# Kernel optimization log

Hardware: AMD Instinct MI355X
Metric: run time of the kernel (lower is better)

## Reference

```python
import jax, jax.numpy as jnp
import numpy as np

jax.config.update("jax_enable_x64", True)

STRIDE = 1
PADDING = 1


def _im2col(x, k, s):
    # x: (n, c, H, W) already padded. Returns (n, c*k*k, oh*ow) with
    # channel-major, then (kh, kw) ordering -- matching torch unfold/img2col.
    n, c, H, W = x.shape
    oh = (H - k) // s + 1
    ow = (W - k) // s + 1
    # k*k = 9 slices: small fixed loop over kernel offsets, fully vectorized
    # over batch/channel/spatial dims.
    patches = jnp.stack(
        [x[:, :, i:i + s * (oh - 1) + 1:s, j:j + s * (ow - 1) + 1:s]
         for i in range(k) for j in range(k)],
        axis=2,
    )  # (n, c, k*k, oh, ow)
    return patches.reshape(n, c * k * k, oh * ow)


def setup_inputs() -> dict:
    key = jax.random.key(0)
    k1, k2, k3 = jax.random.split(key, 3)
    x = jax.random.randint(k1, (32, 64, 56, 56), 0, 65536, dtype=jnp.int64)
    weight = jax.random.randint(k2, (64, 64, 3, 3), 0, 65536, dtype=jnp.int64)
    bias = jax.random.randint(k3, (64,), 0, 65536, dtype=jnp.int64)
    return {"x": x, "weight": weight, "bias": bias}


def reference(x, weight, bias):
    kN, kC, k, _ = weight.shape
    n, c, H, W = x.shape
    oh = (H - k + 2 * PADDING) // STRIDE + 1
    ow = (W - k + 2 * PADDING) // STRIDE + 1
    # pad spatial dims with zeros (ring zero)
    xp = jnp.pad(x, ((0, 0), (0, 0), (PADDING, PADDING), (PADDING, PADDING)))
    cols = _im2col(xp, k, STRIDE)              # (n, c*k*k, L)
    cols_t = cols.transpose(0, 2, 1)           # (n, L, c*k*k)
    w2 = weight.reshape(kN, kC * k * k).T      # (c*k*k, kN)
    # int64 matmul: overflow wraps (two's complement), matching ring Z_{2^64}
    out = jnp.einsum('nlk,ko->nlo', cols_t, w2) + bias  # (n, L, kN)
    return out.transpose(0, 2, 1).reshape(n, kN, oh, ow)
```

## Files before the change

kernel.cpp:

```cpp
#include <hip/hip_runtime.h>


typedef int v4i __attribute__((ext_vector_type(4)));

#define XP   (58 * 58 * 128)
#define ROWB (58 * 128)
#define LCOL 144
#define LROW (58 * LCOL)

__device__ __align__(16) unsigned char g_xp[32 * XP];
__device__ __align__(16) unsigned char g_wb[3 * 9 * 64 * 64];
__device__ unsigned g_off[64];

__global__ __launch_bounds__(256) void packx(const int* __restrict__ x) {
    int gid = blockIdx.x * 256 + threadIdx.x;
    int p  = gid % 3364;
    int r  = gid / 3364;
    int q  = r & 3;
    int n  = r >> 2;
    int pr = p / 58, pc = p - pr * 58;
    int ih = pr - 1, iw = pc - 1;
    unsigned char* ob = g_xp + (long)n * XP + (long)p * 128 + q * 16;
    if ((unsigned)ih < 56u && (unsigned)iw < 56u) {
        const int* xp = x + ((long)(n * 64 + q * 16)) * 3136 + ih * 56 + iw;
        unsigned lo[4], hi[4];
#pragma unroll
        for (int wd = 0; wd < 4; ++wd) {
            unsigned l = 0, h = 0;
#pragma unroll
            for (int j = 0; j < 4; ++j) {
                unsigned v = (unsigned)xp[(long)(wd * 4 + j) * 3136];
                l |= (((v      ) & 0xFFu) ^ 0x80u) << (8 * j);
                h |= (((v >>  8) & 0xFFu) ^ 0x80u) << (8 * j);
            }
            lo[wd] = l; hi[wd] = h;
        }
        *(uint4*)(ob)      = make_uint4(lo[0], lo[1], lo[2], lo[3]);
        *(uint4*)(ob + 64) = make_uint4(hi[0], hi[1], hi[2], hi[3]);
    } else {
        uint4 v = make_uint4(0x80808080u, 0x80808080u, 0x80808080u, 0x80808080u);
        *(uint4*)(ob)      = v;
        *(uint4*)(ob + 64) = v;
    }
}

__global__ __launch_bounds__(256) void packw(const int* __restrict__ w,
                                             const int* __restrict__ bias) {
    int blk = blockIdx.x;
    if (blk < 144) {
        int i = blk * 256 + threadIdx.x;
        if (i >= 64 * 64 * 9) return;
        int k = i / 576;
        int r = i - k * 576;
        int c = r / 9;
        int t = r - c * 9;
        unsigned v = (unsigned)w[i];
        g_wb[((0 * 9 + t) * 64 + k) * 64 + c] = (unsigned char)(v & 127u);
        g_wb[((1 * 9 + t) * 64 + k) * 64 + c] = (unsigned char)((v >> 7) & 127u);
        g_wb[((2 * 9 + t) * 64 + k) * 64 + c] = (unsigned char)((v >> 14) & 3u);
    } else if (threadIdx.x < 64) {
        int k = threadIdx.x;
        unsigned s = 0;
        for (int j = 0; j < 576; ++j) s += (unsigned)w[k * 576 + j];
        g_off[k] = (unsigned)bias[k] + 32896u * s;
    }
}

__global__ __launch_bounds__(256, 3) void secconv(int* __restrict__ out) {
    __shared__ unsigned char sx[4 * LROW];

    const int tid  = threadIdx.x;
    const int blk  = blockIdx.x;
    const int q    = blk >> 3;
    const int rp   = q % 28;
    const int n    = (blk & 7) + 8 * (q / 28);
    const int wid  = tid >> 6;
    const int lane = tid & 63;
    const int lm   = lane & 15;
    const int lq   = lane >> 4;
    const int k0   = wid * 16;

    const unsigned char* gp = g_xp + (long)n * XP + (long)(2 * rp) * ROWB;
#pragma unroll
    for (int s = 0; s < 8; ++s) {
        int i = tid + s * 256;
        if (i < 1856) {
            uint4 v = *(const uint4*)(gp + 16 * i);
            int grow = i / 464;
            int j    = i - grow * 464;
            int gcol = j >> 3, sub = j & 7;
            *(uint4*)(sx + grow * LROW + gcol * LCOL + sub * 16) = v;
        }
    }

    v4i wf0[9], wf1[9], wf2[9];
#pragma unroll
    for (int t = 0; t < 9; ++t) {
        const unsigned char* wb = g_wb + (((t) * 64 + (k0 + lm)) * 64 + lq * 16);
        wf0[t] = *(const v4i*)(wb);
        wf1[t] = *(const v4i*)(wb + 9 * 64 * 64);
        wf2[t] = *(const v4i*)(wb + 18 * 64 * 64);
    }
    unsigned offv[4];
#pragma unroll
    for (int r = 0; r < 4; ++r) offv[r] = g_off[k0 + lq * 4 + r];

    __syncthreads();

    const int r8 = lm >> 3, c8 = lm & 7;
    const unsigned char* lbase = sx + r8 * LROW + c8 * LCOL + lq * 16;

    for (int t = 0; t < 7; ++t) {
        const unsigned char* tb = lbase + t * 8 * LCOL;
        v4i a0 = {0,0,0,0}, a1 = {0,0,0,0}, a2 = {0,0,0,0},
            a3 = {0,0,0,0}, a4 = {0,0,0,0}, a5 = {0,0,0,0};
#pragma unroll
        for (int tap = 0; tap < 9; ++tap) {
            const int dr = tap / 3, dc = tap - (tap / 3) * 3;
            const unsigned char* pp = tb + dr * LROW + dc * LCOL;
            v4i bl = *(const v4i*)(pp);
            v4i bh = *(const v4i*)(pp + 64);
            a0 = __builtin_amdgcn_mfma_i32_16x16x64_i8(wf0[tap], bl, a0, 0, 0, 0);
            a1 = __builtin_amdgcn_mfma_i32_16x16x64_i8(wf0[tap], bh, a1, 0, 0, 0);
            a2 = __builtin_amdgcn_mfma_i32_16x16x64_i8(wf1[tap], bl, a2, 0, 0, 0);
            a3 = __builtin_amdgcn_mfma_i32_16x16x64_i8(wf1[tap], bh, a3, 0, 0, 0);
            a4 = __builtin_amdgcn_mfma_i32_16x16x64_i8(wf2[tap], bl, a4, 0, 0, 0);
            a5 = __builtin_amdgcn_mfma_i32_16x16x64_i8(wf2[tap], bh, a5, 0, 0, 0);
        }

        const long ob = ((long)n * 64 + k0 + lq * 4) * 3136
                      + (long)(2 * rp + r8) * 56 + t * 8 + c8;
#pragma unroll
        for (int r = 0; r < 4; ++r) {
            unsigned val = (unsigned)a0[r]
                         + ((unsigned)a2[r] << 7)
                         + ((unsigned)a1[r] << 8)
                         + ((unsigned)a4[r] << 14)
                         + ((unsigned)a3[r] << 15)
                         + ((unsigned)a5[r] << 22)
                         + offv[r];
            out[ob + (long)r * 3136] = (int)val;
        }
    }
}

extern "C" void kernel_launch(void* const* d_in, const int* in_sizes, int n_in,
                              void* d_out, int out_size, void* d_ws, size_t ws_size,
                              hipStream_t stream)
{
    const int* x    = (const int*)d_in[0];
    const int* w    = (const int*)d_in[1];
    const int* bias = (const int*)d_in[2];
    int* out        = (int*)d_out;

    packx  <<<dim3(1682), dim3(256), 0, stream>>>(x);
    packw  <<<dim3(145),  dim3(256), 0, stream>>>(w, bias);
    secconv<<<dim3(896),  dim3(256), 0, stream>>>(out);
}
```

Before: 117.6 us.

## Use signed 8-bit weight limbs with input-sum correction to cut MFMA count

Splits the weights into two bias-shifted signed 8-bit limbs instead of three unsigned limbs (7/7/2 bits), so each output tile needs four MFMA products per tap instead of six. The cross terms from the bias shift are corrected with a per-pixel input sum (computed in packx and staged in shared memory) plus a per-channel weight-sum offset. Each wave now handles two output-channel tiles over half of the column tiles, which raises register pressure, so the occupancy hint drops from 3 to 2. packx is restructured to produce one pixel's full 64 channels per thread.

```diff
diff --git a/kernel.cpp b/kernel.cpp
--- a/kernel.cpp
+++ b/kernel.cpp
@@ -9,39 +9,51 @@
 #define LROW (58 * LCOL)
 
 __device__ __align__(16) unsigned char g_xp[32 * XP];
-__device__ __align__(16) unsigned char g_wb[3 * 9 * 64 * 64];
+__device__ int g_sp[32 * 3364];
+__device__ __align__(16) unsigned char g_wb[2 * 9 * 64 * 64];
 __device__ unsigned g_off[64];
 
 __global__ __launch_bounds__(256) void packx(const int* __restrict__ x) {
     int gid = blockIdx.x * 256 + threadIdx.x;
-    int p  = gid % 3364;
-    int r  = gid / 3364;
-    int q  = r & 3;
-    int n  = r >> 2;
+    if (gid >= 32 * 3364) return;
+    int p = gid % 3364;
+    int n = gid / 3364;
     int pr = p / 58, pc = p - pr * 58;
     int ih = pr - 1, iw = pc - 1;
-    unsigned char* ob = g_xp + (long)n * XP + (long)p * 128 + q * 16;
+    unsigned char* ob = g_xp + (long)n * XP + (long)p * 128;
+    int S;
     if ((unsigned)ih < 56u && (unsigned)iw < 56u) {
-        const int* xp = x + ((long)(n * 64 + q * 16)) * 3136 + ih * 56 + iw;
-        unsigned lo[4], hi[4];
+        const int* xp = x + (long)n * 64 * 3136 + ih * 56 + iw;
+        unsigned lo[16], hi[16];
+        int s = 0;
 #pragma unroll
-        for (int wd = 0; wd < 4; ++wd) {
+        for (int wd = 0; wd < 16; ++wd) {
             unsigned l = 0, h = 0;
 #pragma unroll
             for (int j = 0; j < 4; ++j) {
                 unsigned v = (unsigned)xp[(long)(wd * 4 + j) * 3136];
+                s += (int)(v & 0xFFFFu);
                 l |= (((v      ) & 0xFFu) ^ 0x80u) << (8 * j);
                 h |= (((v >>  8) & 0xFFu) ^ 0x80u) << (8 * j);
             }
             lo[wd] = l; hi[wd] = h;
         }
-        *(uint4*)(ob)      = make_uint4(lo[0], lo[1], lo[2], lo[3]);
-        *(uint4*)(ob + 64) = make_uint4(hi[0], hi[1], hi[2], hi[3]);
+#pragma unroll
+        for (int q = 0; q < 4; ++q) {
+            *(uint4*)(ob + 16 * q)      = make_uint4(lo[4*q], lo[4*q+1], lo[4*q+2], lo[4*q+3]);
+            *(uint4*)(ob + 64 + 16 * q) = make_uint4(hi[4*q], hi[4*q+1], hi[4*q+2], hi[4*q+3]);
+        }
+        S = s - 2105344;
     } else {
         uint4 v = make_uint4(0x80808080u, 0x80808080u, 0x80808080u, 0x80808080u);
-        *(uint4*)(ob)      = v;
-        *(uint4*)(ob + 64) = v;
+#pragma unroll
+        for (int q = 0; q < 4; ++q) {
+            *(uint4*)(ob + 16 * q)      = v;
+            *(uint4*)(ob + 64 + 16 * q) = v;
+        }
+        S = -2105344;
     }
+    g_sp[gid] = S;
 }
 
 __global__ __launch_bounds__(256) void packw(const int* __restrict__ w,
@@ -55,19 +67,26 @@
         int c = r / 9;
         int t = r - c * 9;
         unsigned v = (unsigned)w[i];
-        g_wb[((0 * 9 + t) * 64 + k) * 64 + c] = (unsigned char)(v & 127u);
-        g_wb[((1 * 9 + t) * 64 + k) * 64 + c] = (unsigned char)((v >> 7) & 127u);
-        g_wb[((2 * 9 + t) * 64 + k) * 64 + c] = (unsigned char)((v >> 14) & 3u);
+        g_wb[((0 * 9 + t) * 64 + k) * 64 + c] = (unsigned char)((v & 255u) ^ 0x80u);
+        g_wb[((1 * 9 + t) * 64 + k) * 64 + c] = (unsigned char)(((v >> 8) & 255u) ^ 0x80u);
     } else if (threadIdx.x < 64) {
         int k = threadIdx.x;
-        unsigned s = 0;
-        for (int j = 0; j < 576; ++j) s += (unsigned)w[k * 576 + j];
-        g_off[k] = (unsigned)bias[k] + 32896u * s;
+        int s0 = 0, s1 = 0;
+        for (int j = 0; j < 576; ++j) {
+            unsigned W = (unsigned)w[k * 576 + j];
+            s0 += (int)(W & 255u);
+            s1 += (int)((W >> 8) & 255u);
+        }
+        s0 -= 73728;
+        s1 -= 73728;
+        unsigned ws = (unsigned)(s0 + 256 * s1);
+        g_off[k] = (unsigned)bias[k] + 32896u * ws + 1082146816u * 576u;
     }
 }
 
-__global__ __launch_bounds__(256, 3) void secconv(int* __restrict__ out) {
+__global__ __launch_bounds__(256, 2) void secconv(int* __restrict__ out) {
     __shared__ unsigned char sx[4 * LROW];
+    __shared__ int ss[4 * 58];
 
     const int tid  = threadIdx.x;
     const int blk  = blockIdx.x;
@@ -78,7 +97,9 @@
     const int lane = tid & 63;
     const int lm   = lane & 15;
     const int lq   = lane >> 4;
-    const int k0   = wid * 16;
+    const int kp   = wid & 1;
+    const int ph   = wid >> 1;
+    const int kbase = kp * 32;
 
     const unsigned char* gp = g_xp + (long)n * XP + (long)(2 * rp) * ROWB;
 #pragma unroll
@@ -92,54 +113,71 @@
             *(uint4*)(sx + grow * LROW + gcol * LCOL + sub * 16) = v;
         }
     }
+    if (tid < 232)
+        ss[tid] = g_sp[n * 3364 + (2 * rp) * 58 + tid];
 
-    v4i wf0[9], wf1[9], wf2[9];
+    v4i wf[2][2][9];
 #pragma unroll
-    for (int t = 0; t < 9; ++t) {
-        const unsigned char* wb = g_wb + (((t) * 64 + (k0 + lm)) * 64 + lq * 16);
-        wf0[t] = *(const v4i*)(wb);
-        wf1[t] = *(const v4i*)(wb + 9 * 64 * 64);
-        wf2[t] = *(const v4i*)(wb + 18 * 64 * 64);
-    }
-    unsigned offv[4];
+    for (int kt = 0; kt < 2; ++kt)
 #pragma unroll
-    for (int r = 0; r < 4; ++r) offv[r] = g_off[k0 + lq * 4 + r];
+        for (int l = 0; l < 2; ++l)
+#pragma unroll
+            for (int t = 0; t < 9; ++t)
+                wf[kt][l][t] = *(const v4i*)(g_wb +
+                    ((l * 9 + t) * 64 + (kbase + kt * 16 + lm)) * 64 + lq * 16);
+    unsigned offv[2][4];
+#pragma unroll
+    for (int kt = 0; kt < 2; ++kt)
+#pragma unroll
+        for (int r = 0; r < 4; ++r)
+            offv[kt][r] = g_off[kbase + kt * 16 + lq * 4 + r];
 
     __syncthreads();
 
     const int r8 = lm >> 3, c8 = lm & 7;
     const unsigned char* lbase = sx + r8 * LROW + c8 * LCOL + lq * 16;
 
-    for (int t = 0; t < 7; ++t) {
+    const int t0 = ph ? 4 : 0, t1 = ph ? 7 : 4;
+    for (int t = t0; t < t1; ++t) {
         const unsigned char* tb = lbase + t * 8 * LCOL;
-        v4i a0 = {0,0,0,0}, a1 = {0,0,0,0}, a2 = {0,0,0,0},
-            a3 = {0,0,0,0}, a4 = {0,0,0,0}, a5 = {0,0,0,0};
+        v4i a00[2] = {{0,0,0,0},{0,0,0,0}}, a01[2] = {{0,0,0,0},{0,0,0,0}};
+        v4i a10[2] = {{0,0,0,0},{0,0,0,0}}, a11[2] = {{0,0,0,0},{0,0,0,0}};
 #pragma unroll
         for (int tap = 0; tap < 9; ++tap) {
             const int dr = tap / 3, dc = tap - (tap / 3) * 3;
             const unsigned char* pp = tb + dr * LROW + dc * LCOL;
             v4i bl = *(const v4i*)(pp);
             v4i bh = *(const v4i*)(pp + 64);
-            a0 = __builtin_amdgcn_mfma_i32_16x16x64_i8(wf0[tap], bl, a0, 0, 0, 0);
-            a1 = __builtin_amdgcn_mfma_i32_16x16x64_i8(wf0[tap], bh, a1, 0, 0, 0);
-            a2 = __builtin_amdgcn_mfma_i32_16x16x64_i8(wf1[tap], bl, a2, 0, 0, 0);
-            a3 = __builtin_amdgcn_mfma_i32_16x16x64_i8(wf1[tap], bh, a3, 0, 0, 0);
-            a4 = __builtin_amdgcn_mfma_i32_16x16x64_i8(wf2[tap], bl, a4, 0, 0, 0);
-            a5 = __builtin_amdgcn_mfma_i32_16x16x64_i8(wf2[tap], bh, a5, 0, 0, 0);
+#pragma unroll
+            for (int kt = 0; kt < 2; ++kt) {
+                a00[kt] = __builtin_amdgcn_mfma_i32_16x16x64_i8(wf[kt][0][tap], bl, a00[kt], 0, 0, 0);
+                a01[kt] = __builtin_amdgcn_mfma_i32_16x16x64_i8(wf[kt][0][tap], bh, a01[kt], 0, 0, 0);
+                a10[kt] = __builtin_amdgcn_mfma_i32_16x16x64_i8(wf[kt][1][tap], bl, a10[kt], 0, 0, 0);
+                a11[kt] = __builtin_amdgcn_mfma_i32_16x16x64_i8(wf[kt][1][tap], bh, a11[kt], 0, 0, 0);
+            }
         }
 
-        const long ob = ((long)n * 64 + k0 + lq * 4) * 3136
-                      + (long)(2 * rp + r8) * 56 + t * 8 + c8;
+        const int pc = t * 8 + c8;
+        int Q = 0;
 #pragma unroll
-        for (int r = 0; r < 4; ++r) {
-            unsigned val = (unsigned)a0[r]
-                         + ((unsigned)a2[r] << 7)
-                         + ((unsigned)a1[r] << 8)
-                         + ((unsigned)a4[r] << 14)
-                         + ((unsigned)a3[r] << 15)
-                         + ((unsigned)a5[r] << 22)
-                         + offv[r];
-            out[ob + (long)r * 3136] = (int)val;
+        for (int dr = 0; dr < 3; ++dr)
+#pragma unroll
+            for (int dc = 0; dc < 3; ++dc)
+                Q += ss[(r8 + dr) * 58 + pc + dc];
+        const unsigned qq = 32896u * (unsigned)Q;
+
+        const long pix = (long)(2 * rp + r8) * 56 + pc;
+#pragma unroll
+        for (int kt = 0; kt < 2; ++kt) {
+            const long ob = ((long)n * 64 + kbase + kt * 16 + lq * 4) * 3136 + pix;
+#pragma unroll
+            for (int r = 0; r < 4; ++r) {
+                unsigned val = (unsigned)a00[kt][r]
+                             + (((unsigned)a01[kt][r] + (unsigned)a10[kt][r]) << 8)
+                             + ((unsigned)a11[kt][r] << 16)
+                             + qq + offv[kt][r];
+                out[ob + (long)r * 3136] = (int)val;
+            }
         }
     }
 }
@@ -153,7 +191,7 @@
     const int* bias = (const int*)d_in[2];
     int* out        = (int*)d_out;
 
-    packx  <<<dim3(1682), dim3(256), 0, stream>>>(x);
-    packw  <<<dim3(145),  dim3(256), 0, stream>>>(w, bias);
-    secconv<<<dim3(896),  dim3(256), 0, stream>>>(out);
+    packx  <<<dim3(421), dim3(256), 0, stream>>>(x);
+    packw  <<<dim3(145), dim3(256), 0, stream>>>(w, bias);
+    secconv<<<dim3(896), dim3(256), 0, stream>>>(out);
 }
```

After: 119.4 us. No clear change (+1.5%).
